# Optimization experiments

Hardware: AMD Instinct MI355X
Metric: run time of the kernel (lower is better)

The kernel has to match this reference:

```python
import jax, jax.numpy as jnp
import numpy as np

B, DIM, S = 8, 512, 1024
H, DH = 8, 64
FF_INNER = 1024      # dim * (ff_mult//2)
CONV_INNER = 1024    # dim * expansion_factor
K = 31
PAD = (K - 1) // 2


def _bn(x, g, b):
    # eval-mode BatchNorm2d with running stats (0,1) absorbed: per-channel affine
    return x * g[None, :, None, None] + b[None, :, None, None]


def _pw(x, w, b):
    # 1x1 Conv2d == channel matmul. x: [B,C,S,1], w: [O,C]
    return jnp.einsum('oc,bcst->bost', w, x) + b[None, :, None, None]


def _ff(x, g, b, w1, b1, w2, b2):
    h = _pw(_bn(x, g, b), w1, b1)
    return _pw(jax.nn.silu(h), w2, b2)


def _attn(x, g, b, wq, bq, wk, bk, wv, bv, wo, bo):
    xn = _bn(x, g, b)
    q = _pw(xn, wq, bq)[..., 0].reshape(B, H, DH, S)
    k = _pw(xn, wk, bk)[..., 0].reshape(B, H, DH, S)
    v = _pw(xn, wv, bv)[..., 0].reshape(B, H, DH, S)
    scale = DH ** -0.5
    scores = jnp.einsum('bhds,bhdt->bhst', q, k) * scale   # [B,H,S,S]
    w = jax.nn.softmax(scores, axis=-1)
    o = jnp.einsum('bhst,bhdt->bhds', w, v).reshape(B, H * DH, S)[..., None]
    return _pw(o, wo, bo)


def _conv(x, g, b, pw1_w, pw1_b, dconv_w, dconv_b, cbn_g, cbn_b, pw2_w, pw2_b):
    h = _pw(_bn(x, g, b), pw1_w, pw1_b)          # [B,2*CONV_INNER,S,1]
    a, gate = jnp.split(h, 2, axis=1)
    h = a * jax.nn.sigmoid(gate)                  # GLU
    h = jnp.transpose(h, (0, 1, 3, 2))            # [B,C,1,S] so kernel (1,K) runs along seq
    h = jax.lax.conv_general_dilated(
        h, dconv_w, window_strides=(1, 1), padding=((0, 0), (PAD, PAD)),
        dimension_numbers=('NCHW', 'OIHW', 'NCHW'))
    h = jnp.transpose(h, (0, 1, 3, 2)) + dconv_b[None, :, None, None]
    h = jax.nn.silu(_bn(h, cbn_g, cbn_b))
    return _pw(h, pw2_w, pw2_b)


def setup_inputs() -> dict:
    key = jax.random.key(0)
    ks = iter(jax.random.split(key, 32))
    w = lambda *s: jax.random.normal(next(ks), s, jnp.float32) * 0.02
    d = {
        'x': jax.random.normal(next(ks), (B, DIM, S, 1), jnp.float32),
        'ff1_g': jnp.ones((DIM,)), 'ff1_b': jnp.zeros((DIM,)),
        'ff1_w1': w(FF_INNER, DIM), 'ff1_b1': jnp.zeros((FF_INNER,)),
        'ff1_w2': w(DIM, FF_INNER), 'ff1_b2': jnp.zeros((DIM,)),
        'attn_g': jnp.ones((DIM,)), 'attn_b': jnp.zeros((DIM,)),
        'wq': w(H * DH, DIM), 'bq': jnp.zeros((H * DH,)),
        'wk': w(H * DH, DIM), 'bk': jnp.zeros((H * DH,)),
        'wv': w(H * DH, DIM), 'bv': jnp.zeros((H * DH,)),
        'wo': w(DIM, H * DH), 'bo': jnp.zeros((DIM,)),
        'conv_g': jnp.ones((DIM,)), 'conv_b': jnp.zeros((DIM,)),
        'pw1_w': w(2 * CONV_INNER, DIM), 'pw1_b': jnp.zeros((2 * CONV_INNER,)),
        'dconv_w': w(CONV_INNER, CONV_INNER, 1, K), 'dconv_b': jnp.zeros((CONV_INNER,)),
        'cbn_g': jnp.ones((CONV_INNER,)), 'cbn_b': jnp.zeros((CONV_INNER,)),
        'pw2_w': w(DIM, CONV_INNER), 'pw2_b': jnp.zeros((DIM,)),
        'ff2_g': jnp.ones((DIM,)), 'ff2_b': jnp.zeros((DIM,)),
        'ff2_w1': w(FF_INNER, DIM), 'ff2_b1': jnp.zeros((FF_INNER,)),
        'ff2_w2': w(DIM, FF_INNER), 'ff2_b2': jnp.zeros((DIM,)),
        'fin_g': jnp.ones((DIM,)), 'fin_b': jnp.zeros((DIM,)),
    }
    return d


def reference(x, ff1_g, ff1_b, ff1_w1, ff1_b1, ff1_w2, ff1_b2,
              attn_g, attn_b, wq, bq, wk, bk, wv, bv, wo, bo,
              conv_g, conv_b, pw1_w, pw1_b, dconv_w, dconv_b, cbn_g, cbn_b, pw2_w, pw2_b,
              ff2_g, ff2_b, ff2_w1, ff2_b1, ff2_w2, ff2_b2, fin_g, fin_b):
    x1 = x + 0.5 * _ff(x, ff1_g, ff1_b, ff1_w1, ff1_b1, ff1_w2, ff1_b2)
    x2 = x1 + _attn(x1, attn_g, attn_b, wq, bq, wk, bk, wv, bv, wo, bo)
    x3 = x2 + _conv(x2, conv_g, conv_b, pw1_w, pw1_b, dconv_w, dconv_b, cbn_g, cbn_b, pw2_w, pw2_b)
    x4 = x3 + 0.5 * _ff(x3, ff2_g, ff2_b, ff2_w1, ff2_b1, ff2_w2, ff2_b2)
    return _bn(x4, fin_g, fin_b)
```

## Files before the change

### kernel.cpp

```cpp
#include <hip/hip_runtime.h>
#include <cstdint>
#include <cstddef>

using bf16 = __bf16;
typedef __bf16 bf16x8 __attribute__((ext_vector_type(8)));
typedef float f32x4 __attribute__((ext_vector_type(4)));
typedef unsigned int uint4v __attribute__((ext_vector_type(4)));

#define NB 8
#define DIM 512
#define SEQ 1024
#define NH 8
#define DH 64
#define CONV_INNER 1024
#define KW 31
#define PADW 15
#define HPRA 1056

__device__ __forceinline__ float fsigmoid(float x) { return 1.f / (1.f + __expf(-x)); }
__device__ __forceinline__ float fsilu(float x) { return x * fsigmoid(x); }

__device__ __forceinline__ void gld16(const bf16* g, bf16* l) {
  __builtin_amdgcn_global_load_lds(
      (const __attribute__((address_space(1))) unsigned int*)g,
      (__attribute__((address_space(3))) unsigned int*)l, 16, 0, 0);
}


__global__ __launch_bounds__(256) void k_diag(float* __restrict__ out, int n, float v) {
  int i = blockIdx.x * 256 + threadIdx.x;
  if (i < n) out[i] = v;
}


__global__ __launch_bounds__(256) void k_convert_bf16(const float* __restrict__ src,
                                                      bf16* __restrict__ dst, int n) {
  int i = (blockIdx.x * 256 + threadIdx.x) * 4;
  if (i + 3 < n) {
    float4 v = *reinterpret_cast<const float4*>(src + i);
    dst[i]     = (bf16)v.x;
    dst[i + 1] = (bf16)v.y;
    dst[i + 2] = (bf16)v.z;
    dst[i + 3] = (bf16)v.w;
  }
}

__global__ __launch_bounds__(256) void k_conv_wt(const float* __restrict__ w,
                                                 bf16* __restrict__ wt) {
  __shared__ float t[256 * KW];
  int o = blockIdx.x, i0 = blockIdx.y * 256;
  const float* src = w + (size_t)o * (CONV_INNER * KW) + (size_t)i0 * KW;
  for (int idx = threadIdx.x; idx < 256 * KW; idx += 256) t[idx] = src[idx];
  __syncthreads();
  for (int k = 0; k < KW; ++k) {
    wt[((size_t)k * CONV_INNER + o) * CONV_INNER + i0 + threadIdx.x] =
        (bf16)t[threadIdx.x * KW + k];
  }
}

__global__ __launch_bounds__(256) void k_pad_zero(bf16* __restrict__ hpad) {
  int i = blockIdx.x * 256 + threadIdx.x;
  int b = i / (32 * 128);
  int r = (i >> 7) & 31;
  int c8 = (i & 127) * 8;
  int row = (r < PADW) ? r : 1024 + r;
  uint4v z = {0u, 0u, 0u, 0u};
  *reinterpret_cast<uint4v*>(&hpad[((size_t)b * HPRA + row) * CONV_INNER + c8]) = z;
}

__global__ __launch_bounds__(256) void k_transpose_in(const float* __restrict__ x,
                                                      const float* __restrict__ g,
                                                      const float* __restrict__ bvec,
                                                      float* __restrict__ xT,
                                                      bf16* __restrict__ xbn) {
  __shared__ float t[32][33];
  int s0 = blockIdx.x * 32, c0 = blockIdx.y * 32, b = blockIdx.z;
  int col = threadIdx.x & 31, rq = threadIdx.x >> 5;
#pragma unroll
  for (int i = 0; i < 4; ++i) {
    int row = rq + i * 8;
    t[row][col] = x[((size_t)b * DIM + c0 + row) * SEQ + s0 + col];
  }
  __syncthreads();
  float gg = g[c0 + col], bb = bvec[c0 + col];
#pragma unroll
  for (int i = 0; i < 4; ++i) {
    int srow = rq + i * 8;
    float v = t[col][srow];
    size_t off = ((size_t)b * SEQ + s0 + srow) * DIM + c0 + col;
    xT[off] = v;
    xbn[off] = (bf16)(v * gg + bb);
  }
}

__global__ __launch_bounds__(256) void k_concat_bias(const float* __restrict__ bq,
                                                     const float* __restrict__ bk,
                                                     const float* __restrict__ bv,
                                                     float* __restrict__ qb) {
  int i = blockIdx.x * 256 + threadIdx.x;
  if (i < 512) qb[i] = bq[i];
  else if (i < 1024) qb[i] = bk[i - 512];
  else if (i < 1536) qb[i] = bv[i - 1024];
}

template <int EPI>
__global__ __launch_bounds__(256) void k_gemm(const bf16* __restrict__ A,
                                              const bf16* __restrict__ W,
                                              const float* __restrict__ bias,
                                              const float* __restrict__ res,
                                              const float* __restrict__ g,
                                              const float* __restrict__ bb,
                                              float* __restrict__ outf,
                                              bf16* __restrict__ outb, int N, int K) {
  __shared__ __align__(16) bf16 sA[2][128 * 64];
  __shared__ __align__(16) bf16 sB[2][128 * 64];
  const int tid = threadIdx.x;
  const int b = blockIdx.z;
  const int m0 = blockIdx.y * 128, n0 = blockIdx.x * 128;
  const int lane = tid & 63, wid = tid >> 6;
  const int wm = (wid & 1) * 64, wn = (wid >> 1) * 64;
  const int fr = lane & 15, fg = lane >> 4;
  const int srow = lane >> 3;
  const int scol = ((lane & 7) ^ srow) * 8;

  f32x4 acc[4][4];
#pragma unroll
  for (int i = 0; i < 4; ++i)
#pragma unroll
    for (int j = 0; j < 4; ++j) acc[i][j] = (f32x4)0.f;

  const bf16* Abase = A + ((size_t)b * SEQ + m0 + srow) * K + scol;
  const bf16* Wbase = W + (size_t)(n0 + srow) * K + scol;
  const int nch = K >> 6;

#pragma unroll
  for (int c = 0; c < 4; ++c) {
    const int ch = wid + c * 4;
    gld16(Abase + (size_t)(ch * 8) * K, &sA[0][ch * 512]);
    gld16(Wbase + (size_t)(ch * 8) * K, &sB[0][ch * 512]);
  }
  __syncthreads();

  int buf = 0;
  for (int kt = 0; kt < nch; ++kt) {
    if (kt + 1 < nch) {
      const int kc = (kt + 1) * 64;
#pragma unroll
      for (int c = 0; c < 4; ++c) {
        const int ch = wid + c * 4;
        gld16(Abase + (size_t)(ch * 8) * K + kc, &sA[buf ^ 1][ch * 512]);
        gld16(Wbase + (size_t)(ch * 8) * K + kc, &sB[buf ^ 1][ch * 512]);
      }
    }
#pragma unroll
    for (int kk = 0; kk < 2; ++kk) {
      const int cg = kk * 4 + fg;
      bf16x8 aF[4], bF[4];
#pragma unroll
      for (int i = 0; i < 4; ++i) {
        const int ar = wm + i * 16 + fr;
        aF[i] = *reinterpret_cast<const bf16x8*>(
            &sA[buf][ar * 64 + ((cg ^ (ar & 7)) * 8)]);
        const int br = wn + i * 16 + fr;
        bF[i] = *reinterpret_cast<const bf16x8*>(
            &sB[buf][br * 64 + ((cg ^ (br & 7)) * 8)]);
      }
#pragma unroll
      for (int mi = 0; mi < 4; ++mi)
#pragma unroll
        for (int ni = 0; ni < 4; ++ni)
          acc[mi][ni] = __builtin_amdgcn_mfma_f32_16x16x32_bf16(aF[mi], bF[ni],
                                                                acc[mi][ni], 0, 0, 0);
    }
    __syncthreads();
    buf ^= 1;
  }

#pragma unroll
  for (int mi = 0; mi < 4; ++mi) {
#pragma unroll
    for (int ni = 0; ni < 4; ++ni) {
      int ncol = n0 + wn + ni * 16 + fr;
      float bv = bias[ncol];
      if constexpr (EPI == 5) {
        float gg = g[ncol], bbv = bb[ncol];
        int mrow0 = m0 + wm + mi * 16 + fg * 4;
        float v[4];
#pragma unroll
        for (int j = 0; j < 4; ++j) {
          float a = acc[mi][ni][j] + bv;
          float r = res[((size_t)b * SEQ + mrow0 + j) * 512 + ncol] + 0.5f * a;
          v[j] = r * gg + bbv;
        }
        *reinterpret_cast<float4*>(outf + ((size_t)b * 512 + ncol) * SEQ + mrow0) =
            make_float4(v[0], v[1], v[2], v[3]);
      } else {
#pragma unroll
        for (int j = 0; j < 4; ++j) {
          int mrow = m0 + wm + mi * 16 + fg * 4 + j;
          size_t off = ((size_t)b * SEQ + mrow) * N + ncol;
          float a = acc[mi][ni][j] + bv;
          if constexpr (EPI == 0) {
            outb[off] = (bf16)fsilu(a);
          } else if constexpr (EPI == 2) {
            outb[off] = (bf16)a;
          } else if constexpr (EPI == 1) {
            float r = res[off] + 0.5f * a;
            outf[off] = r;
            outb[off] = (bf16)(r * g[ncol] + bb[ncol]);
          } else if constexpr (EPI == 3) {
            float r = res[off] + a;
            outf[off] = r;
            outb[off] = (bf16)(r * g[ncol] + bb[ncol]);
          }
        }
      }
    }
  }
}

__global__ __launch_bounds__(256) void k_pw1_glu(const bf16* __restrict__ A,
                                                 const bf16* __restrict__ W,
                                                 const float* __restrict__ bias,
                                                 bf16* __restrict__ hpad) {
  __shared__ __align__(16) bf16 sA[128][40];
  __shared__ __align__(16) bf16 sBa[128][40];
  __shared__ __align__(16) bf16 sBg[128][40];
  const int tid = threadIdx.x;
  const int b = blockIdx.z;
  const int m0 = blockIdx.y * 128, n0 = blockIdx.x * 128;
  const int lane = tid & 63, wid = tid >> 6;
  const int wm = (wid & 1) * 64, wn = (wid >> 1) * 64;
  const int fr = lane & 15, fg = lane >> 4;
  const int K = 512;

  f32x4 accA[4][4], accG[4][4];
#pragma unroll
  for (int i = 0; i < 4; ++i)
#pragma unroll
    for (int j = 0; j < 4; ++j) { accA[i][j] = (f32x4)0.f; accG[i][j] = (f32x4)0.f; }

  const int srow = tid >> 1, sc = (tid & 1) * 16;
  const bf16* Abase = A + ((size_t)b * SEQ + m0 + srow) * K + sc;
  const bf16* WaB = W + (size_t)(n0 + srow) * K + sc;
  const bf16* WgB = W + (size_t)(n0 + 1024 + srow) * K + sc;

  for (int kt = 0; kt < K; kt += 32) {
    uint4v a0 = *reinterpret_cast<const uint4v*>(Abase + kt);
    uint4v a1 = *reinterpret_cast<const uint4v*>(Abase + kt + 8);
    uint4v wa0 = *reinterpret_cast<const uint4v*>(WaB + kt);
    uint4v wa1 = *reinterpret_cast<const uint4v*>(WaB + kt + 8);
    uint4v wg0 = *reinterpret_cast<const uint4v*>(WgB + kt);
    uint4v wg1 = *reinterpret_cast<const uint4v*>(WgB + kt + 8);
    *reinterpret_cast<uint4v*>(&sA[srow][sc]) = a0;
    *reinterpret_cast<uint4v*>(&sA[srow][sc + 8]) = a1;
    *reinterpret_cast<uint4v*>(&sBa[srow][sc]) = wa0;
    *reinterpret_cast<uint4v*>(&sBa[srow][sc + 8]) = wa1;
    *reinterpret_cast<uint4v*>(&sBg[srow][sc]) = wg0;
    *reinterpret_cast<uint4v*>(&sBg[srow][sc + 8]) = wg1;
    __syncthreads();
    bf16x8 aF[4], bFa[4], bFg[4];
#pragma unroll
    for (int i = 0; i < 4; ++i) {
      aF[i]  = *reinterpret_cast<const bf16x8*>(&sA[wm + i * 16 + fr][fg * 8]);
      bFa[i] = *reinterpret_cast<const bf16x8*>(&sBa[wn + i * 16 + fr][fg * 8]);
      bFg[i] = *reinterpret_cast<const bf16x8*>(&sBg[wn + i * 16 + fr][fg * 8]);
    }
#pragma unroll
    for (int mi = 0; mi < 4; ++mi)
#pragma unroll
      for (int ni = 0; ni < 4; ++ni) {
        accA[mi][ni] =
            __builtin_amdgcn_mfma_f32_16x16x32_bf16(aF[mi], bFa[ni], accA[mi][ni], 0, 0, 0);
        accG[mi][ni] =
            __builtin_amdgcn_mfma_f32_16x16x32_bf16(aF[mi], bFg[ni], accG[mi][ni], 0, 0, 0);
      }
    __syncthreads();
  }

#pragma unroll
  for (int mi = 0; mi < 4; ++mi) {
#pragma unroll
    for (int ni = 0; ni < 4; ++ni) {
      int ncol = n0 + wn + ni * 16 + fr;
      float ba = bias[ncol], bg = bias[ncol + 1024];
#pragma unroll
      for (int j = 0; j < 4; ++j) {
        int mrow = m0 + wm + mi * 16 + fg * 4 + j;
        float av = accA[mi][ni][j] + ba;
        float gv = accG[mi][ni][j] + bg;
        hpad[((size_t)b * HPRA + PADW + mrow) * CONV_INNER + ncol] =
            (bf16)(av * fsigmoid(gv));
      }
    }
  }
}

__global__ __launch_bounds__(256) void k_conv(const bf16* __restrict__ hpad,
                                              const bf16* __restrict__ wt,
                                              const float* __restrict__ bias,
                                              const float* __restrict__ g,
                                              const float* __restrict__ bb,
                                              bf16* __restrict__ outb) {
  __shared__ __align__(16) bf16 sA[160 * 64];
  __shared__ __align__(16) bf16 sB0[128 * 64];
  __shared__ __align__(16) bf16 sB1[128 * 64];
  const int tid = threadIdx.x;
  const int b = blockIdx.z;
  const int n0 = blockIdx.x * 128, m0 = blockIdx.y * 128;
  const int lane = tid & 63, wid = tid >> 6;
  const int wm = (wid & 1) * 64, wn = (wid >> 1) * 64;
  const int fr = lane & 15, fg = lane >> 4;
  const int srow = lane >> 3;
  const int scol = ((lane & 7) ^ srow) * 8;

  f32x4 acc[4][4];
#pragma unroll
  for (int i = 0; i < 4; ++i)
#pragma unroll
    for (int j = 0; j < 4; ++j) acc[i][j] = (f32x4)0.f;

  const bf16* Abase = hpad + ((size_t)b * HPRA + m0 + srow) * CONV_INNER + scol;
  const bf16* Wbase = wt + (size_t)(n0 + srow) * CONV_INNER + scol;

  for (int it = 0; it < 16; ++it) {
    const int itc = it * 64;
#pragma unroll
    for (int c = 0; c < 5; ++c) {
      const int ch = wid + c * 4;
      gld16(Abase + (size_t)(ch * 8) * CONV_INNER + itc, &sA[ch * 512]);
    }
#pragma unroll
    for (int c = 0; c < 4; ++c) {
      const int ch = wid + c * 4;
      gld16(Wbase + (size_t)(ch * 8) * CONV_INNER + itc, &sB0[ch * 512]);
    }
    __syncthreads();

    for (int ks = 0; ks < KW; ++ks) {
      const bf16* cur = (ks & 1) ? sB1 : sB0;
      bf16* nxt = (ks & 1) ? sB0 : sB1;
      if (ks + 1 < KW) {
#pragma unroll
        for (int c = 0; c < 4; ++c) {
          const int ch = wid + c * 4;
          gld16(Wbase + (size_t)(ks + 1) * CONV_INNER * CONV_INNER +
                    (size_t)(ch * 8) * CONV_INNER + itc,
                &nxt[ch * 512]);
        }
      }
#pragma unroll
      for (int kk = 0; kk < 2; ++kk) {
        const int cg = kk * 4 + fg;
        bf16x8 aF[4], bF[4];
#pragma unroll
        for (int i = 0; i < 4; ++i) {
          const int ar = ks + wm + i * 16 + fr;
          aF[i] = *reinterpret_cast<const bf16x8*>(
              &sA[ar * 64 + ((cg ^ (ar & 7)) * 8)]);
        }
#pragma unroll
        for (int n = 0; n < 4; ++n) {
          const int br = wn + n * 16 + fr;
          bF[n] = *reinterpret_cast<const bf16x8*>(
              &cur[br * 64 + ((cg ^ (br & 7)) * 8)]);
        }
#pragma unroll
        for (int mi = 0; mi < 4; ++mi)
#pragma unroll
          for (int ni = 0; ni < 4; ++ni)
            acc[mi][ni] = __builtin_amdgcn_mfma_f32_16x16x32_bf16(aF[mi], bF[ni],
                                                                  acc[mi][ni], 0, 0, 0);
      }
      __syncthreads();
    }
  }

#pragma unroll
  for (int mi = 0; mi < 4; ++mi) {
#pragma unroll
    for (int ni = 0; ni < 4; ++ni) {
      int ncol = n0 + wn + ni * 16 + fr;
      float bv = bias[ncol], gg = g[ncol], bbv = bb[ncol];
#pragma unroll
      for (int j = 0; j < 4; ++j) {
        int mrow = m0 + wm + mi * 16 + fg * 4 + j;
        float a = acc[mi][ni][j] + bv;
        outb[((size_t)b * SEQ + mrow) * CONV_INNER + ncol] = (bf16)fsilu(a * gg + bbv);
      }
    }
  }
}

__global__ __launch_bounds__(256) void k_attn(const bf16* __restrict__ qkv,
                                              bf16* __restrict__ out) {
  __shared__ __align__(16) bf16 sQ[128][72];
  __shared__ __align__(16) bf16 sK[64][72];
  __shared__ __align__(16) bf16 sVT[64][72];
  __shared__ __align__(16) bf16 sP[128][72];
  const int tid = threadIdx.x;
  const int bh = blockIdx.y;
  const int b = bh >> 3, h = bh & 7;
  const int m0 = blockIdx.x * 128;
  const int lane = tid & 63, wid = tid >> 6;
  const int w32 = wid * 32;
  const int fr = lane & 15, fg = lane >> 4;
  const size_t base = (size_t)b * SEQ * 1536;

  for (int idx = tid; idx < 128 * 8; idx += 256) {
    int row = idx >> 3, c = (idx & 7) * 8;
    *reinterpret_cast<uint4v*>(&sQ[row][c]) =
        *reinterpret_cast<const uint4v*>(qkv + base + (size_t)(m0 + row) * 1536 + h * 64 + c);
  }

  f32x4 o[2][4];
  float mst[2][4], lst[2][4];
#pragma unroll
  for (int mi = 0; mi < 2; ++mi)
#pragma unroll
    for (int j = 0; j < 4; ++j) {
      mst[mi][j] = -1e30f;
      lst[mi][j] = 0.f;
#pragma unroll
      for (int df = 0; df < 4; ++df) o[mi][df] = (f32x4)0.f;
    }

  for (int t0 = 0; t0 < SEQ; t0 += 64) {
    for (int idx = tid; idx < 64 * 8; idx += 256) {
      int row = idx >> 3, c = (idx & 7) * 8;
      *reinterpret_cast<uint4v*>(&sK[row][c]) = *reinterpret_cast<const uint4v*>(
          qkv + base + (size_t)(t0 + row) * 1536 + 512 + h * 64 + c);
    }
    for (int e = tid; e < 64 * 64; e += 256) {
      int t = e >> 6, d = e & 63;
      sVT[d][t] = qkv[base + (size_t)(t0 + t) * 1536 + 1024 + h * 64 + d];
    }
    __syncthreads();

    f32x4 sacc[2][4];
#pragma unroll
    for (int mi = 0; mi < 2; ++mi)
#pragma unroll
      for (int tf = 0; tf < 4; ++tf) sacc[mi][tf] = (f32x4)0.f;
#pragma unroll
    for (int kk = 0; kk < 2; ++kk) {
      bf16x8 aQ[2], bK[4];
#pragma unroll
      for (int mi = 0; mi < 2; ++mi)
        aQ[mi] = *reinterpret_cast<const bf16x8*>(&sQ[w32 + mi * 16 + fr][kk * 32 + fg * 8]);
#pragma unroll
      for (int tf = 0; tf < 4; ++tf)
        bK[tf] = *reinterpret_cast<const bf16x8*>(&sK[tf * 16 + fr][kk * 32 + fg * 8]);
#pragma unroll
      for (int mi = 0; mi < 2; ++mi)
#pragma unroll
        for (int tf = 0; tf < 4; ++tf)
          sacc[mi][tf] =
              __builtin_amdgcn_mfma_f32_16x16x32_bf16(aQ[mi], bK[tf], sacc[mi][tf], 0, 0, 0);
    }

#pragma unroll
    for (int mi = 0; mi < 2; ++mi) {
#pragma unroll
      for (int j = 0; j < 4; ++j) {
        float rm = -1e30f;
#pragma unroll
        for (int tf = 0; tf < 4; ++tf) rm = fmaxf(rm, sacc[mi][tf][j] * 0.125f);
#pragma unroll
        for (int off = 1; off < 16; off <<= 1) rm = fmaxf(rm, __shfl_xor(rm, off));
        float mnew = fmaxf(mst[mi][j], rm);
        float al = __expf(mst[mi][j] - mnew);
        float ps = 0.f;
#pragma unroll
        for (int tf = 0; tf < 4; ++tf) {
          float p = __expf(sacc[mi][tf][j] * 0.125f - mnew);
          ps += p;
          sP[w32 + mi * 16 + fg * 4 + j][tf * 16 + fr] = (bf16)p;
        }
#pragma unroll
        for (int off = 1; off < 16; off <<= 1) ps += __shfl_xor(ps, off);
        lst[mi][j] = lst[mi][j] * al + ps;
        mst[mi][j] = mnew;
#pragma unroll
        for (int df = 0; df < 4; ++df) o[mi][df][j] *= al;
      }
    }
    __syncthreads();

#pragma unroll
    for (int kk = 0; kk < 2; ++kk) {
      bf16x8 aP[2], bV[4];
#pragma unroll
      for (int mi = 0; mi < 2; ++mi)
        aP[mi] = *reinterpret_cast<const bf16x8*>(&sP[w32 + mi * 16 + fr][kk * 32 + fg * 8]);
#pragma unroll
      for (int df = 0; df < 4; ++df)
        bV[df] = *reinterpret_cast<const bf16x8*>(&sVT[df * 16 + fr][kk * 32 + fg * 8]);
#pragma unroll
      for (int mi = 0; mi < 2; ++mi)
#pragma unroll
        for (int df = 0; df < 4; ++df)
          o[mi][df] = __builtin_amdgcn_mfma_f32_16x16x32_bf16(aP[mi], bV[df], o[mi][df], 0, 0, 0);
    }
    __syncthreads();
  }

#pragma unroll
  for (int mi = 0; mi < 2; ++mi)
#pragma unroll
    for (int df = 0; df < 4; ++df)
#pragma unroll
      for (int j = 0; j < 4; ++j) {
        int row = m0 + w32 + mi * 16 + fg * 4 + j;
        int col = h * 64 + df * 16 + fr;
        out[((size_t)b * SEQ + row) * 512 + col] = (bf16)(o[mi][df][j] / lst[mi][j]);
      }
}


extern "C" void kernel_launch(void* const* d_in, const int* in_sizes, int n_in,
                              void* d_out, int out_size, void* d_ws, size_t ws_size,
                              hipStream_t stream) {
  const float* x      = (const float*)d_in[0];
  const float* ff1_g  = (const float*)d_in[1];
  const float* ff1_b  = (const float*)d_in[2];
  const float* ff1_w1 = (const float*)d_in[3];
  const float* ff1_b1 = (const float*)d_in[4];
  const float* ff1_w2 = (const float*)d_in[5];
  const float* ff1_b2 = (const float*)d_in[6];
  const float* attn_g = (const float*)d_in[7];
  const float* attn_b = (const float*)d_in[8];
  const float* wq     = (const float*)d_in[9];
  const float* bq     = (const float*)d_in[10];
  const float* wk     = (const float*)d_in[11];
  const float* bk     = (const float*)d_in[12];
  const float* wv     = (const float*)d_in[13];
  const float* bv     = (const float*)d_in[14];
  const float* wo     = (const float*)d_in[15];
  const float* bo     = (const float*)d_in[16];
  const float* conv_g = (const float*)d_in[17];
  const float* conv_b = (const float*)d_in[18];
  const float* pw1_w  = (const float*)d_in[19];
  const float* pw1_b  = (const float*)d_in[20];
  const float* dconv_w = (const float*)d_in[21];
  const float* dconv_b = (const float*)d_in[22];
  const float* cbn_g  = (const float*)d_in[23];
  const float* cbn_b  = (const float*)d_in[24];
  const float* pw2_w  = (const float*)d_in[25];
  const float* pw2_b  = (const float*)d_in[26];
  const float* ff2_g  = (const float*)d_in[27];
  const float* ff2_b  = (const float*)d_in[28];
  const float* ff2_w1 = (const float*)d_in[29];
  const float* ff2_b1 = (const float*)d_in[30];
  const float* ff2_w2 = (const float*)d_in[31];
  const float* ff2_b2 = (const float*)d_in[32];
  const float* fin_g  = (const float*)d_in[33];
  const float* fin_b  = (const float*)d_in[34];

  char* ws = (char*)d_ws;
  size_t off = 0;
  auto alloc = [&](size_t bytes) -> void* {
    off = (off + 255) & ~(size_t)255;
    void* p = ws + off;
    off += bytes;
    return p;
  };

  bf16* wqkv  = (bf16*)alloc((size_t)1536 * 512 * 2);
  float* qkvb = (float*)alloc(1536 * 4);
  bf16* wf1a  = (bf16*)alloc((size_t)1024 * 512 * 2);
  bf16* wf1b  = (bf16*)alloc((size_t)512 * 1024 * 2);
  bf16* wwo   = (bf16*)alloc((size_t)512 * 512 * 2);
  bf16* wpw1  = (bf16*)alloc((size_t)2048 * 512 * 2);
  bf16* wpw2  = (bf16*)alloc((size_t)512 * 1024 * 2);
  bf16* wf2a  = (bf16*)alloc((size_t)1024 * 512 * 2);
  bf16* wf2b  = (bf16*)alloc((size_t)512 * 1024 * 2);

  bf16*  Bn  = (bf16*)alloc((size_t)NB * SEQ * 512 * 2);
  float* F1  = (float*)alloc((size_t)NB * SEQ * 512 * 4);
  bf16*  HGp = (bf16*)alloc((size_t)NB * HPRA * 1024 * 2);
  bf16*  H2  = (bf16*)alloc((size_t)NB * SEQ * 1024 * 2);

  char* E = (char*)alloc((size_t)KW * 1024 * 1024 * 2);
  bf16*  wt     = (bf16*)E;
  bf16*  h1     = (bf16*)E;
  bf16*  qkv    = (bf16*)E;
  bf16*  attn_o = (bf16*)(E + (size_t)24 * 1024 * 1024);
  float* x1     = (float*)(E + (size_t)32 * 1024 * 1024);
  float* x3     = (float*)E;
  bf16*  h3     = (bf16*)(E + (size_t)16 * 1024 * 1024);

  float* xT = F1;
  float* x2 = F1;
  bf16* xbn = Bn, *x1bn = Bn, *x2bn = Bn, *x3bn = Bn;
  size_t needed = off;
  (void)in_sizes; (void)n_in;

  if (ws_size < needed) {
    k_diag<<<(out_size + 255) / 256, 256, 0, stream>>>(
        (float*)d_out, out_size, (float)(ws_size >> 20));
    return;
  }

  auto cvt = [&](const float* s, bf16* d, int n) {
    k_convert_bf16<<<n / 1024, 256, 0, stream>>>(s, d, n);
  };
  cvt(wq, wqkv, 512 * 512);
  cvt(wk, wqkv + 512 * 512, 512 * 512);
  cvt(wv, wqkv + 1024 * 512, 512 * 512);
  cvt(ff1_w1, wf1a, 1024 * 512);
  cvt(ff1_w2, wf1b, 512 * 1024);
  cvt(wo, wwo, 512 * 512);
  cvt(pw1_w, wpw1, 2048 * 512);
  cvt(pw2_w, wpw2, 512 * 1024);
  cvt(ff2_w1, wf2a, 1024 * 512);
  cvt(ff2_w2, wf2b, 512 * 1024);
  k_concat_bias<<<6, 256, 0, stream>>>(bq, bk, bv, qkvb);
  k_pad_zero<<<(NB * 32 * 128) / 256, 256, 0, stream>>>(HGp);
  k_transpose_in<<<dim3(32, 16, NB), 256, 0, stream>>>(x, ff1_g, ff1_b, xT, xbn);

  k_gemm<0><<<dim3(8, 8, NB), 256, 0, stream>>>(xbn, wf1a, ff1_b1, nullptr, nullptr,
                                                nullptr, nullptr, h1, 1024, 512);
  k_gemm<1><<<dim3(4, 8, NB), 256, 0, stream>>>(h1, wf1b, ff1_b2, xT, attn_g, attn_b,
                                                x1, x1bn, 512, 1024);
  k_gemm<2><<<dim3(12, 8, NB), 256, 0, stream>>>(x1bn, wqkv, qkvb, nullptr, nullptr,
                                                 nullptr, nullptr, qkv, 1536, 512);
  k_attn<<<dim3(8, 64), 256, 0, stream>>>(qkv, attn_o);
  k_gemm<3><<<dim3(4, 8, NB), 256, 0, stream>>>(attn_o, wwo, bo, x1, conv_g, conv_b,
                                                x2, x2bn, 512, 512);
  k_conv_wt<<<dim3(1024, 4), 256, 0, stream>>>(dconv_w, wt);
  k_pw1_glu<<<dim3(8, 8, NB), 256, 0, stream>>>(x2bn, wpw1, pw1_b, HGp);
  k_conv<<<dim3(8, 8, NB), 256, 0, stream>>>(HGp, wt, dconv_b, cbn_g, cbn_b, H2);
  k_gemm<3><<<dim3(4, 8, NB), 256, 0, stream>>>(H2, wpw2, pw2_b, x2, ff2_g, ff2_b,
                                                x3, x3bn, 512, 1024);
  k_gemm<0><<<dim3(8, 8, NB), 256, 0, stream>>>(x3bn, wf2a, ff2_b1, nullptr, nullptr,
                                                nullptr, nullptr, h3, 1024, 512);
  k_gemm<5><<<dim3(4, 8, NB), 256, 0, stream>>>(h3, wf2b, ff2_b2, x3, fin_g, fin_b,
                                                (float*)d_out, nullptr, 512, 1024);
}
```

Measured before the change: 786.0 us.

## Triple-buffer conv weight loads and switch pw1 GLU to async LDS loads

The depthwise-style conv kernel moves from double to triple buffering of weight tiles, prefetching two kernel taps ahead. It uses explicit vmcnt waits in place of full syncthreads so that global loads overlap with MFMA work. The pw1+GLU GEMM replaces register-staged 32-wide K tiles with direct global_load_lds of 64-wide swizzled tiles, which halves the number of barriers and avoids the register round-trip. The cost is more LDS per block, which may lower occupancy. The hand-written vmcnt counts must also exactly match the number of outstanding loads.

```diff
diff --git a/kernel.cpp b/kernel.cpp
--- a/kernel.cpp
+++ b/kernel.cpp
@@ -223,15 +223,17 @@
                                                  const bf16* __restrict__ W,
                                                  const float* __restrict__ bias,
                                                  bf16* __restrict__ hpad) {
-  __shared__ __align__(16) bf16 sA[128][40];
-  __shared__ __align__(16) bf16 sBa[128][40];
-  __shared__ __align__(16) bf16 sBg[128][40];
+  __shared__ __align__(16) bf16 sA[128 * 64];
+  __shared__ __align__(16) bf16 sBa[128 * 64];
+  __shared__ __align__(16) bf16 sBg[128 * 64];
   const int tid = threadIdx.x;
   const int b = blockIdx.z;
   const int m0 = blockIdx.y * 128, n0 = blockIdx.x * 128;
   const int lane = tid & 63, wid = tid >> 6;
   const int wm = (wid & 1) * 64, wn = (wid >> 1) * 64;
   const int fr = lane & 15, fg = lane >> 4;
+  const int srow = lane >> 3;
+  const int scol = ((lane & 7) ^ srow) * 8;
   const int K = 512;
 
   f32x4 accA[4][4], accG[4][4];
@@ -240,41 +242,45 @@
 #pragma unroll
     for (int j = 0; j < 4; ++j) { accA[i][j] = (f32x4)0.f; accG[i][j] = (f32x4)0.f; }
 
-  const int srow = tid >> 1, sc = (tid & 1) * 16;
-  const bf16* Abase = A + ((size_t)b * SEQ + m0 + srow) * K + sc;
-  const bf16* WaB = W + (size_t)(n0 + srow) * K + sc;
-  const bf16* WgB = W + (size_t)(n0 + 1024 + srow) * K + sc;
-
-  for (int kt = 0; kt < K; kt += 32) {
-    uint4v a0 = *reinterpret_cast<const uint4v*>(Abase + kt);
-    uint4v a1 = *reinterpret_cast<const uint4v*>(Abase + kt + 8);
-    uint4v wa0 = *reinterpret_cast<const uint4v*>(WaB + kt);
-    uint4v wa1 = *reinterpret_cast<const uint4v*>(WaB + kt + 8);
-    uint4v wg0 = *reinterpret_cast<const uint4v*>(WgB + kt);
-    uint4v wg1 = *reinterpret_cast<const uint4v*>(WgB + kt + 8);
-    *reinterpret_cast<uint4v*>(&sA[srow][sc]) = a0;
-    *reinterpret_cast<uint4v*>(&sA[srow][sc + 8]) = a1;
-    *reinterpret_cast<uint4v*>(&sBa[srow][sc]) = wa0;
-    *reinterpret_cast<uint4v*>(&sBa[srow][sc + 8]) = wa1;
-    *reinterpret_cast<uint4v*>(&sBg[srow][sc]) = wg0;
-    *reinterpret_cast<uint4v*>(&sBg[srow][sc + 8]) = wg1;
+  const bf16* Abase = A + ((size_t)b * SEQ + m0 + srow) * K + scol;
+  const bf16* WaB = W + (size_t)(n0 + srow) * K + scol;
+  const bf16* WgB = W + (size_t)(n0 + 1024 + srow) * K + scol;
+
+  for (int kt = 0; kt < 8; ++kt) {
+    const int kc = kt * 64;
+#pragma unroll
+    for (int c = 0; c < 4; ++c) {
+      const int ch = wid + c * 4;
+      gld16(Abase + (size_t)(ch * 8) * K + kc, &sA[ch * 512]);
+      gld16(WaB + (size_t)(ch * 8) * K + kc, &sBa[ch * 512]);
+      gld16(WgB + (size_t)(ch * 8) * K + kc, &sBg[ch * 512]);
+    }
     __syncthreads();
-    bf16x8 aF[4], bFa[4], bFg[4];
-#pragma unroll
-    for (int i = 0; i < 4; ++i) {
-      aF[i]  = *reinterpret_cast<const bf16x8*>(&sA[wm + i * 16 + fr][fg * 8]);
-      bFa[i] = *reinterpret_cast<const bf16x8*>(&sBa[wn + i * 16 + fr][fg * 8]);
-      bFg[i] = *reinterpret_cast<const bf16x8*>(&sBg[wn + i * 16 + fr][fg * 8]);
-    }
-#pragma unroll
-    for (int mi = 0; mi < 4; ++mi)
-#pragma unroll
-      for (int ni = 0; ni < 4; ++ni) {
-        accA[mi][ni] =
-            __builtin_amdgcn_mfma_f32_16x16x32_bf16(aF[mi], bFa[ni], accA[mi][ni], 0, 0, 0);
-        accG[mi][ni] =
-            __builtin_amdgcn_mfma_f32_16x16x32_bf16(aF[mi], bFg[ni], accG[mi][ni], 0, 0, 0);
-      }
+#pragma unroll
+    for (int kk = 0; kk < 2; ++kk) {
+      const int cg = kk * 4 + fg;
+      bf16x8 aF[4], bFa[4], bFg[4];
+#pragma unroll
+      for (int i = 0; i < 4; ++i) {
+        const int ar = wm + i * 16 + fr;
+        aF[i] = *reinterpret_cast<const bf16x8*>(
+            &sA[ar * 64 + ((cg ^ (ar & 7)) * 8)]);
+        const int br = wn + i * 16 + fr;
+        bFa[i] = *reinterpret_cast<const bf16x8*>(
+            &sBa[br * 64 + ((cg ^ (br & 7)) * 8)]);
+        bFg[i] = *reinterpret_cast<const bf16x8*>(
+            &sBg[br * 64 + ((cg ^ (br & 7)) * 8)]);
+      }
+#pragma unroll
+      for (int mi = 0; mi < 4; ++mi)
+#pragma unroll
+        for (int ni = 0; ni < 4; ++ni) {
+          accA[mi][ni] =
+              __builtin_amdgcn_mfma_f32_16x16x32_bf16(aF[mi], bFa[ni], accA[mi][ni], 0, 0, 0);
+          accG[mi][ni] =
+              __builtin_amdgcn_mfma_f32_16x16x32_bf16(aF[mi], bFg[ni], accG[mi][ni], 0, 0, 0);
+        }
+    }
     __syncthreads();
   }
 
@@ -303,8 +309,7 @@
                                               const float* __restrict__ bb,
                                               bf16* __restrict__ outb) {
   __shared__ __align__(16) bf16 sA[160 * 64];
-  __shared__ __align__(16) bf16 sB0[128 * 64];
-  __shared__ __align__(16) bf16 sB1[128 * 64];
+  __shared__ __align__(16) bf16 sBb[3][128 * 64];
   const int tid = threadIdx.x;
   const int b = blockIdx.z;
   const int n0 = blockIdx.x * 128, m0 = blockIdx.y * 128;
@@ -313,6 +318,7 @@
   const int fr = lane & 15, fg = lane >> 4;
   const int srow = lane >> 3;
   const int scol = ((lane & 7) ^ srow) * 8;
+  const size_t WKS = (size_t)CONV_INNER * CONV_INNER;
 
   f32x4 acc[4][4];
 #pragma unroll
@@ -333,20 +339,26 @@
 #pragma unroll
     for (int c = 0; c < 4; ++c) {
       const int ch = wid + c * 4;
-      gld16(Wbase + (size_t)(ch * 8) * CONV_INNER + itc, &sB0[ch * 512]);
-    }
-    __syncthreads();
-
+      gld16(Wbase + (size_t)(ch * 8) * CONV_INNER + itc, &sBb[0][ch * 512]);
+    }
+#pragma unroll
+    for (int c = 0; c < 4; ++c) {
+      const int ch = wid + c * 4;
+      gld16(Wbase + WKS + (size_t)(ch * 8) * CONV_INNER + itc, &sBb[1][ch * 512]);
+    }
+    asm volatile("s_waitcnt vmcnt(4)" ::: "memory");
+    __builtin_amdgcn_s_barrier();
+
+    const bf16* bcur = sBb[0];
+    const bf16* bnext = sBb[1];
+    bf16* bfill = sBb[2];
     for (int ks = 0; ks < KW; ++ks) {
-      const bf16* cur = (ks & 1) ? sB1 : sB0;
-      bf16* nxt = (ks & 1) ? sB0 : sB1;
-      if (ks + 1 < KW) {
+      if (ks + 2 < KW) {
 #pragma unroll
         for (int c = 0; c < 4; ++c) {
           const int ch = wid + c * 4;
-          gld16(Wbase + (size_t)(ks + 1) * CONV_INNER * CONV_INNER +
-                    (size_t)(ch * 8) * CONV_INNER + itc,
-                &nxt[ch * 512]);
+          gld16(Wbase + (size_t)(ks + 2) * WKS + (size_t)(ch * 8) * CONV_INNER + itc,
+                bfill + ch * 512);
         }
       }
 #pragma unroll
@@ -363,7 +375,7 @@
         for (int n = 0; n < 4; ++n) {
           const int br = wn + n * 16 + fr;
           bF[n] = *reinterpret_cast<const bf16x8*>(
-              &cur[br * 64 + ((cg ^ (br & 7)) * 8)]);
+              &bcur[br * 64 + ((cg ^ (br & 7)) * 8)]);
         }
 #pragma unroll
         for (int mi = 0; mi < 4; ++mi)
@@ -372,7 +384,16 @@
             acc[mi][ni] = __builtin_amdgcn_mfma_f32_16x16x32_bf16(aF[mi], bF[ni],
                                                                   acc[mi][ni], 0, 0, 0);
       }
-      __syncthreads();
+      if (ks + 2 < KW) {
+        asm volatile("s_waitcnt vmcnt(4)" ::: "memory");
+      } else {
+        asm volatile("s_waitcnt vmcnt(0)" ::: "memory");
+      }
+      __builtin_amdgcn_s_barrier();
+      const bf16* t = bcur;
+      bcur = bnext;
+      bnext = bfill;
+      bfill = (bf16*)t;
     }
   }
 
```

Result: slower. 802.4 us (+2.1%).
